# Kernel tuning notes

Hardware: AMD Instinct MI355X
Metric: run time of the kernel (lower is better)

The kernel has to match this reference:

```python
import jax, jax.numpy as jnp
import numpy as np
from jax import lax

DN = ('NCHW', 'OIHW', 'NCHW')

def _conv(x, w, pad):
    return lax.conv_general_dilated(x, w, (1, 1), pad, dimension_numbers=DN)

def _bn(x, p, eps=1e-5):
    # p: [4, C] rows = gamma, beta, mean, var ; inference-mode batchnorm
    g, b, m, v = p[0], p[1], p[2], p[3]
    scale = g / jnp.sqrt(v + eps)
    return (x - m[:, None, None]) * scale[:, None, None] + b[:, None, None]

def setup_inputs() -> dict:
    key = jax.random.key(0)
    ks = jax.random.split(key, 12)
    B, C, H, W = 16, 512, 56, 56
    mid = C // 2
    def bn_params(k):
        k1, k2, k3, k4 = jax.random.split(k, 4)
        g = 1.0 + 0.1 * jax.random.normal(k1, (mid,), jnp.float32)
        b = 0.1 * jax.random.normal(k2, (mid,), jnp.float32)
        m = 0.1 * jax.random.normal(k3, (mid,), jnp.float32)
        v = 0.5 + jax.random.uniform(k4, (mid,), jnp.float32)
        return jnp.stack([g, b, m, v])
    return {
        'x': jax.random.normal(ks[0], (B, C, H, W), jnp.float32),
        'w_main': 0.03 * jax.random.normal(ks[1], (mid, C, 3, 3), jnp.float32),
        'w_1x1': 0.05 * jax.random.normal(ks[2], (mid, C, 1, 1), jnp.float32),
        'w31': 0.05 * jax.random.normal(ks[3], (mid, C, 1, 1), jnp.float32),
        'bn31': bn_params(ks[4]),
        'w33': 0.05 * jax.random.normal(ks[5], (mid, mid, 3, 3), jnp.float32),
        'bn33': bn_params(ks[6]),
        'wa1': 0.05 * jax.random.normal(ks[7], (mid, C, 1, 1), jnp.float32),
        'bna1': bn_params(ks[8]),
        'bna2': bn_params(ks[9]),
        'fuse_weight': jnp.ones((4,), jnp.float32),
        'c_score': jax.random.normal(ks[10], (2 * C,), jnp.float32),
    }

def reference(x, w_main, w_1x1, w31, bn31, w33, bn33, wa1, bna1, bna2, fuse_weight, c_score):
    c = x.shape[1]
    # four branches (note: forward applies BN only inside the 3x3 and avg branches)
    acs_main = _conv(x * fuse_weight[0], w_main, 'SAME')
    acs_1x1 = _conv(x * fuse_weight[1], w_1x1, 'VALID')
    acs_3x3 = _bn(_conv(_bn(_conv(x * fuse_weight[2], w31, 'VALID'), bn31), w33, 'SAME'), bn33)
    avg_in = _bn(_conv(x * fuse_weight[3], wa1, 'VALID'), bna1)
    # AvgPool2d(k=3, s=1, p=1, count_include_pad=True)
    pooled = lax.reduce_window(avg_in, 0.0, lax.add, (1, 1, 3, 3), (1, 1, 1, 1),
                               [(0, 0), (0, 0), (1, 1), (1, 1)]) / 9.0
    acs_avg = _bn(pooled, bna2)
    out = jnp.concatenate([acs_main, acs_1x1, acs_3x3, acs_avg], axis=1)  # [B, 2c, H, W]
    # sparse 1x1 selection: output channel i = input channel ind[i] * sigmoid(c_score[ind[i]])
    _, ind = lax.top_k(c_score, c)
    scale = jax.nn.sigmoid(c_score)[ind]  # [c]
    out = out[:, ind] * scale[None, :, None, None]
    return out
```

## Files before the change

kernel.cpp:

```cpp
#include <hip/hip_runtime.h>
#include <hip/hip_bf16.h>
#include <cstdint>
#include <cstddef>

typedef _Float16 f16x8_t __attribute__((ext_vector_type(8)));
typedef float    f32x4_t __attribute__((ext_vector_type(4)));
typedef unsigned short u16x8_t __attribute__((ext_vector_type(8)));
typedef unsigned short u16x4_t __attribute__((ext_vector_type(4)));

__device__ __forceinline__ unsigned short f2h(float f) {
    return __builtin_bit_cast(unsigned short, (_Float16)f);
}
__device__ __forceinline__ float h2f(unsigned short h) {
    return (float)__builtin_bit_cast(_Float16, h);
}
__device__ __forceinline__ f16x8_t load_h8(const unsigned short* p) {
    u16x8_t r = *(const u16x8_t*)p;
    return __builtin_bit_cast(f16x8_t, r);
}

#define BATCH 16
#define CFULL 512
#define CMID  256
#define HW    3136
#define WDIM  56

#define POS_STRIDE_SH 40
#define LDS_SHORTS (348 * 40)

__global__ void prep_tabs(const float* __restrict__ cscore,
                          const float* __restrict__ bn31, const float* __restrict__ bn33,
                          const float* __restrict__ bna1, const float* __restrict__ bna2,
                          int* __restrict__ pos_tab, float* __restrict__ scale_tab,
                          float* __restrict__ bnab)
{
    __shared__ float s[1024];
    int t = threadIdx.x;
    s[t] = cscore[t];
    __syncthreads();
    float sj = s[t];
    int cnt = 0;
    for (int k = 0; k < 1024; ++k) {
        float sk = s[k];
        cnt += (sk > sj) || (sk == sj && k < t);
    }
    pos_tab[t]   = (cnt < 512) ? cnt : -1;
    scale_tab[t] = 1.0f / (1.0f + expf(-sj));

    if (t < 256) {
        const float* srcs[4] = {bn31, bn33, bna1, bna2};
        #pragma unroll
        for (int q = 0; q < 4; ++q) {
            const float* sp = srcs[q];
            float g = sp[t], b = sp[256 + t], m = sp[512 + t], v = sp[768 + t];
            float a = g * rsqrtf(v + 1e-5f);
            bnab[q * 512 + t]       = a;
            bnab[q * 512 + 256 + t] = b - m * a;
        }
    }
}

__global__ void prep_weights(const float* __restrict__ w_main, const float* __restrict__ w_1x1,
                             const float* __restrict__ w31, const float* __restrict__ wa1,
                             const float* __restrict__ w33, const float* __restrict__ fw,
                             unsigned short* __restrict__ Wcat,
                             unsigned short* __restrict__ Wmain,
                             unsigned short* __restrict__ W33r)
{
    int i = blockIdx.x * 256 + threadIdx.x;
    if (i < 393216) {
        int row = i >> 9, c = i & 511;
        float v;
        if (row < 256)      v = w_1x1[row * 512 + c] * fw[1];
        else if (row < 512) v = w31[(row - 256) * 512 + c] * fw[2];
        else                v = wa1[(row - 512) * 512 + c] * fw[3];
        Wcat[((c >> 5) * 768 + row) * 32 + (c & 31)] = f2h(v);
    } else if (i < 393216 + 1179648) {
        int j = i - 393216;
        int o = j / 4608, r = j % 4608, tap = r >> 9, c = r & 511;
        Wmain[(((c >> 5) * 9 + tap) * 256 + o) * 32 + (c & 31)] =
            f2h(w_main[(size_t)(o * 512 + c) * 9 + tap] * fw[0]);
    } else if (i < 2162688) {
        int j = i - 1572864;
        int o = j / 2304, r = j % 2304, tap = r >> 8, c = r & 255;
        W33r[(((c >> 5) * 9 + tap) * 256 + o) * 32 + (c & 31)] =
            f2h(w33[(size_t)(o * 256 + c) * 9 + tap]);
    }
}

__global__ void transpose_x(const float* __restrict__ x, unsigned short* __restrict__ xt)
{
    __shared__ unsigned short tile[64][65];
    int t = threadIdx.x;
    int hw0 = blockIdx.x * 64, c0 = blockIdx.y * 64, b = blockIdx.z;
    const float* xb = x + ((size_t)b * CFULL + c0) * HW + hw0;
    int hwL = t & 63, cL = t >> 6;
    #pragma unroll
    for (int i = 0; i < 16; ++i) {
        int c = cL + i * 4;
        tile[c][hwL] = f2h(xb[(size_t)c * HW + hwL]);
    }
    __syncthreads();
    int c8 = (t & 7) * 8, hw = t >> 3;
    #pragma unroll
    for (int i = 0; i < 2; ++i) {
        int hh = hw + i * 32;
        u16x8_t v;
        #pragma unroll
        for (int j = 0; j < 8; ++j) v[j] = tile[c8 + j][hh];
        *(u16x8_t*)(xt + ((size_t)b * HW + hw0 + hh) * CFULL + c0 + c8) = v;
    }
}

template<int CIN, int NTAP, int MODE>
__device__ __forceinline__ void conv_body(
    const unsigned short* __restrict__ X,
    const unsigned short* __restrict__ Wr,
    float* __restrict__ out,
    unsigned short* __restrict__ u_dst,
    unsigned short* __restrict__ avg_dst,
    const float* __restrict__ bnab,
    const int* __restrict__ pos_tab,
    const float* __restrict__ scale_tab,
    unsigned short* smem, int b, int ob, int pb)
{
    const int t    = threadIdx.x;
    const int lane = t & 63;
    const int wid  = t >> 6;
    const int wm = wid >> 1, wn = wid & 1;
    const int lr = lane & 15;
    const int ko = (lane >> 4) * 8;
    const int row0 = pb * 4;

    const int o_wave = ob * 128 + wm * 64;
    const int p_wave = pb * 224 + wn * 112;

    int bofs[7];
    #pragma unroll
    for (int n = 0; n < 7; ++n) {
        int p = p_wave + n * 16 + lr;
        bofs[n] = ((p / WDIM - row0) * 58 + p % WDIM) * POS_STRIDE_SH + ko;
    }

    const int r_lo = (NTAP == 9) ? 0 : 1;
    const int nitems = ((NTAP == 9) ? 6 : 4) * 224;
    int  s_src[6];
    int  s_dst[6];
    bool s_val[6];
    #pragma unroll
    for (int i = 0; i < 6; ++i) {
        int idx = t + i * 256;
        bool act = idx < nitems;
        int r   = r_lo + idx / 224;
        int rm  = idx % 224;
        int col = rm >> 2, sub = rm & 3;
        int ir  = row0 + r - 1;
        s_val[i] = act && ((unsigned)ir < (unsigned)WDIM);
        s_src[i] = (ir * WDIM + col) * CIN + sub * 8;
        s_dst[i] = (r * 58 + col + 1) * POS_STRIDE_SH + sub * 8;
    }

    #pragma unroll
    for (int i = 0; i < 7; ++i) {
        int j = t + i * 256;
        if (j < LDS_SHORTS / 8)
            *(u16x8_t*)(smem + j * 8) = (u16x8_t){0, 0, 0, 0, 0, 0, 0, 0};
    }

    f32x4_t acc[4][7];
    #pragma unroll
    for (int m = 0; m < 4; ++m)
        #pragma unroll
        for (int n = 0; n < 7; ++n)
            acc[m][n] = (f32x4_t){0.f, 0.f, 0.f, 0.f};

    const int astep = (MODE == 1) ? 768 * 32 : 256 * 32;
    const unsigned short* am[4];
    #pragma unroll
    for (int m = 0; m < 4; ++m)
        am[m] = Wr + (size_t)(o_wave + m * 16 + lr) * 32 + ko;

    const unsigned short* xb = X + (size_t)b * HW * CIN;
    const int KCH = CIN / 32;

    for (int kch = 0; kch < KCH; ++kch) {
        __syncthreads();
        u16x8_t buf[6];
        #pragma unroll
        for (int i = 0; i < 6; ++i)
            if (s_val[i]) buf[i] = *(const u16x8_t*)(xb + s_src[i] + kch * 32);
        #pragma unroll
        for (int i = 0; i < 6; ++i)
            if (s_val[i]) *(u16x8_t*)(smem + s_dst[i]) = buf[i];
        __syncthreads();

        #pragma unroll
        for (int tap = 0; tap < NTAP; ++tap) {
            const int toff = (NTAP == 9) ? (((tap / 3) * 58 + tap % 3) * POS_STRIDE_SH)
                                         : (59 * POS_STRIDE_SH);
            f16x8_t af[4];
            #pragma unroll
            for (int m = 0; m < 4; ++m)
                af[m] = load_h8(am[m] + (size_t)(kch * NTAP + tap) * astep);
            f16x8_t bf[7];
            #pragma unroll
            for (int n = 0; n < 7; ++n)
                bf[n] = load_h8(smem + bofs[n] + toff);
            __builtin_amdgcn_s_setprio(1);
            #pragma unroll
            for (int m = 0; m < 4; ++m)
                #pragma unroll
                for (int n = 0; n < 7; ++n)
                    acc[m][n] = __builtin_amdgcn_mfma_f32_16x16x32_f16(af[m], bf[n], acc[m][n], 0, 0, 0);
            __builtin_amdgcn_s_setprio(0);
        }
    }

    const int fq = lane >> 4;
    const int seg = (MODE == 1) ? (ob >> 1) : 0;
    const bool bn_write = (MODE == 1) && (seg != 0);

    #pragma unroll
    for (int m = 0; m < 4; ++m) {
        const int orow = o_wave + m * 16 + fq * 4;
        #pragma unroll
        for (int n = 0; n < 7; ++n) {
            const int p = p_wave + n * 16 + lr;
            f32x4_t v = acc[m][n];
            if (bn_write) {
                const int lc0 = orow - seg * 256;
                const float* ab = (seg == 1) ? (bnab + 0 * 512) : (bnab + 2 * 512);
                unsigned short* dst = (seg == 1) ? u_dst : avg_dst;
                u16x4_t pk;
                #pragma unroll
                for (int j = 0; j < 4; ++j) {
                    float a = ab[lc0 + j], bb = ab[256 + lc0 + j];
                    pk[j] = f2h(a * v[j] + bb);
                }
                *(u16x4_t*)(dst + ((size_t)b * HW + p) * CMID + lc0) = pk;
            } else {
                const int cbase = (MODE == 0) ? 0 : ((MODE == 2) ? 512 : 256);
                #pragma unroll
                for (int j = 0; j < 4; ++j) {
                    int o = orow + j;
                    float val2 = v[j];
                    if (MODE == 2) val2 = bnab[512 + o] * val2 + bnab[512 + 256 + o];
                    int jc = cbase + o;
                    int pos = pos_tab[jc];
                    if (pos >= 0)
                        out[((size_t)b * CFULL + pos) * HW + p] = val2 * scale_tab[jc];
                }
            }
        }
    }
}

__global__ __launch_bounds__(256, 2)
void fusedK(const unsigned short* __restrict__ X,
            const unsigned short* __restrict__ Wcat,
            float* __restrict__ out,
            unsigned short* __restrict__ u_dst,
            unsigned short* __restrict__ avg_dst,
            const float* __restrict__ bnab,
            const int* __restrict__ pos_tab,
            const float* __restrict__ scale_tab)
{
    __shared__ unsigned short smem[LDS_SHORTS];
    const int id = blockIdx.x;
    const int xcd = id & 7, slot = id >> 3;
    const int b = xcd + 8 * (slot / 84);
    const int u = slot % 84;
    conv_body<512, 1, 1>(X, Wcat, out, u_dst, avg_dst, bnab,
                         pos_tab, scale_tab, smem, b, u / 14, u % 14);
}

__global__ __launch_bounds__(256, 2)
void longK(const unsigned short* __restrict__ X,
           const unsigned short* __restrict__ Wmain,
           const unsigned short* __restrict__ U,
           const unsigned short* __restrict__ W33r,
           const unsigned short* __restrict__ avgin,
           float* __restrict__ out,
           const float* __restrict__ bnab,
           const int* __restrict__ pos_tab,
           const float* __restrict__ scale_tab)
{
    __shared__ unsigned short smem[LDS_SHORTS];
    const int id = blockIdx.x;
    const int xcd = id & 7, slot = id >> 3;
    if (slot < 112) {
        const int b = xcd + 8 * (slot / 56);
        const int rr = slot % 56;
        const int idx = rr >> 1;
        const int ob = idx / 14, pb = idx % 14;
        if ((rr & 1) == 0)
            conv_body<512, 9, 0>(X, Wmain, out, nullptr, nullptr, bnab,
                                 pos_tab, scale_tab, smem, b, ob, pb);
        else
            conv_body<256, 9, 2>(U, W33r, out, nullptr, nullptr, bnab,
                                 pos_tab, scale_tab, smem, b, ob, pb);
    } else {
        const int s2 = slot - 112;
        const int b = xcd + 8 * (s2 / 392);
        const int q = s2 % 392;
        const int t = threadIdx.x;
        const int p = q * 8 + (t >> 5);
        const int c0 = (t & 31) * 8;
        const int h = p / WDIM, w = p % WDIM;
        const float* ab2 = bnab + 3 * 512;
        float s[8];
        #pragma unroll
        for (int j = 0; j < 8; ++j) s[j] = 0.f;
        #pragma unroll
        for (int dh = -1; dh <= 1; ++dh) {
            int hh = h + dh;
            if ((unsigned)hh >= (unsigned)WDIM) continue;
            #pragma unroll
            for (int dw = -1; dw <= 1; ++dw) {
                int ww = w + dw;
                if ((unsigned)ww >= (unsigned)WDIM) continue;
                u16x8_t v = *(const u16x8_t*)(avgin + ((size_t)b * HW + hh * WDIM + ww) * CMID + c0);
                #pragma unroll
                for (int j = 0; j < 8; ++j) s[j] += h2f(v[j]);
            }
        }
        #pragma unroll
        for (int j = 0; j < 8; ++j) {
            int c = c0 + j;
            int jc = 768 + c;
            int pos = pos_tab[jc];
            if (pos >= 0) {
                float val = (s[j] * (1.f / 9.f)) * ab2[c] + ab2[256 + c];
                out[((size_t)b * CFULL + pos) * HW + p] = val * scale_tab[jc];
            }
        }
    }
}

extern "C" void kernel_launch(void* const* d_in, const int* in_sizes, int n_in,
                              void* d_out, int out_size, void* d_ws, size_t ws_size,
                              hipStream_t stream) {
    (void)in_sizes; (void)n_in; (void)out_size; (void)ws_size;
    const float* x      = (const float*)d_in[0];
    const float* w_main = (const float*)d_in[1];
    const float* w_1x1  = (const float*)d_in[2];
    const float* w31    = (const float*)d_in[3];
    const float* bn31   = (const float*)d_in[4];
    const float* w33    = (const float*)d_in[5];
    const float* bn33   = (const float*)d_in[6];
    const float* wa1    = (const float*)d_in[7];
    const float* bna1   = (const float*)d_in[8];
    const float* bna2   = (const float*)d_in[9];
    const float* fw     = (const float*)d_in[10];
    const float* cscore = (const float*)d_in[11];
    float* out = (float*)d_out;

    char* ws = (char*)d_ws;
    unsigned short* x_nhwc = (unsigned short*)(ws);
    unsigned short* u_nhwc = (unsigned short*)(ws + 51380224);
    unsigned short* avgin  = (unsigned short*)(ws + 77070336);
    unsigned short* Wcat   = (unsigned short*)(ws + 102760448);
    unsigned short* Wmain  = (unsigned short*)(ws + 103546880);
    unsigned short* W33r   = (unsigned short*)(ws + 105906176);
    float*          bnab   = (float*)        (ws + 107085824);
    int*            pos_tab= (int*)          (ws + 107094016);
    float*          scl_tab= (float*)        (ws + 107098112);

    dim3 blk(256);

    prep_tabs<<<dim3(1), dim3(1024), 0, stream>>>(cscore, bn31, bn33, bna1, bna2,
                                                  pos_tab, scl_tab, bnab);
    prep_weights<<<dim3(8448), blk, 0, stream>>>(w_main, w_1x1, w31, wa1, w33, fw,
                                                 Wcat, Wmain, W33r);
    transpose_x<<<dim3(49, 8, 16), blk, 0, stream>>>(x, x_nhwc);

    fusedK<<<dim3(1344), blk, 0, stream>>>(x_nhwc, Wcat, out,
                                           u_nhwc, avgin, bnab, pos_tab, scl_tab);

    longK<<<dim3(7168), blk, 0, stream>>>(x_nhwc, Wmain, u_nhwc, W33r, avgin,
                                          out, bnab, pos_tab, scl_tab);
}
```

Measured before the change: 435.9 us.

## Add double-buffered software-pipelined 3x3 conv path with prefetched weights

Adds a new conv_sched routine for the two 3x3 convolutions in longK. It double-buffers the input halo tile in LDS and prefetches the next channel chunk into registers during tap 7. It also register-prefetches the next tap's weight fragments and uses explicit waitcnt, sched_barrier and setprio so the MFMAs overlap the loads. The longK LDS allocation doubles plus a dump region, which may cut occupancy below the two blocks per CU requested.

```diff
diff --git a/kernel.cpp b/kernel.cpp
--- a/kernel.cpp
+++ b/kernel.cpp
@@ -255,6 +255,161 @@
     }
 }
 
+template<int CIN, int MODE>
+__device__ __forceinline__ void conv_sched(
+    const unsigned short* __restrict__ X,
+    const unsigned short* __restrict__ Wr,
+    float* __restrict__ out,
+    const float* __restrict__ bnab,
+    const int* __restrict__ pos_tab,
+    const float* __restrict__ scale_tab,
+    unsigned short* smem, int b, int ob, int pb)
+{
+    const int t    = threadIdx.x;
+    const int lane = t & 63;
+    const int wid  = t >> 6;
+    const int wm = wid >> 1, wn = wid & 1;
+    const int lr = lane & 15;
+    const int ko = (lane >> 4) * 8;
+    const int row0 = pb * 4;
+
+    const int o_wave = ob * 128 + wm * 64;
+    const int p_wave = pb * 224 + wn * 112;
+
+    int bofs[7];
+    #pragma unroll
+    for (int n = 0; n < 7; ++n) {
+        int p = p_wave + n * 16 + lr;
+        bofs[n] = ((p / WDIM - row0) * 58 + p % WDIM) * POS_STRIDE_SH + ko;
+    }
+
+    const int nitems = 6 * 224;
+    const int dump_off = 2 * LDS_SHORTS + (t & 63) * 8 + (wid & 3) * 512;
+    int s_src[6];
+    int s_dst[6];
+    #pragma unroll
+    for (int i = 0; i < 6; ++i) {
+        int idx = t + i * 256;
+        int r   = idx / 224;
+        int rm  = idx % 224;
+        int col = rm >> 2, sub = rm & 3;
+        int ir  = row0 + r - 1;
+        bool v  = (idx < nitems) && ((unsigned)ir < (unsigned)WDIM);
+        int ir_c = v ? ir : 0;
+        s_src[i] = (ir_c * WDIM + col) * CIN + sub * 8;
+        s_dst[i] = v ? ((r * 58 + col + 1) * POS_STRIDE_SH + sub * 8) : dump_off;
+    }
+
+    #pragma unroll
+    for (int i = 0; i < 14; ++i) {
+        int j = t + i * 256;
+        if (j < 2 * LDS_SHORTS / 8)
+            *(u16x8_t*)(smem + j * 8) = (u16x8_t){0, 0, 0, 0, 0, 0, 0, 0};
+    }
+
+    f32x4_t acc[4][7];
+    #pragma unroll
+    for (int m = 0; m < 4; ++m)
+        #pragma unroll
+        for (int n = 0; n < 7; ++n)
+            acc[m][n] = (f32x4_t){0.f, 0.f, 0.f, 0.f};
+
+    const int astep = 256 * 32;
+    const unsigned short* am[4];
+    #pragma unroll
+    for (int m = 0; m < 4; ++m)
+        am[m] = Wr + (size_t)(o_wave + m * 16 + lr) * 32 + ko;
+
+    const unsigned short* xb = X + (size_t)b * HW * CIN;
+    const int KCH = CIN / 32;
+
+    u16x8_t sbuf[6];
+    __syncthreads();
+    #pragma unroll
+    for (int i = 0; i < 6; ++i)
+        sbuf[i] = *(const u16x8_t*)(xb + s_src[i]);
+    asm volatile("s_waitcnt vmcnt(0)" ::: "memory");
+    #pragma unroll
+    for (int i = 0; i < 6; ++i)
+        *(u16x8_t*)(smem + s_dst[i]) = sbuf[i];
+    f16x8_t afc[4], afn[4];
+    #pragma unroll
+    for (int m = 0; m < 4; ++m)
+        afc[m] = load_h8(am[m]);
+    asm volatile("s_waitcnt lgkmcnt(0)" ::: "memory");
+    __builtin_amdgcn_s_barrier();
+
+    #pragma unroll 1
+    for (int kch = 0; kch < KCH; ++kch) {
+        const unsigned short* rbuf = smem + (kch & 1) * LDS_SHORTS;
+        unsigned short* wbuf = smem + ((kch + 1) & 1) * LDS_SHORTS;
+        const int nk = (kch + 1 < KCH) ? (kch + 1) : 0;
+
+        #pragma unroll
+        for (int tap = 0; tap < 9; ++tap) {
+            int kt = kch * 9 + tap + 1;
+            kt = (kt == KCH * 9) ? 0 : kt;
+            #pragma unroll
+            for (int m = 0; m < 4; ++m)
+                afn[m] = load_h8(am[m] + (size_t)kt * astep);
+            if (tap == 7) {
+                #pragma unroll
+                for (int i = 0; i < 6; ++i)
+                    sbuf[i] = *(const u16x8_t*)(xb + s_src[i] + nk * 32);
+            }
+            const int toff = ((tap / 3) * 58 + tap % 3) * POS_STRIDE_SH;
+            f16x8_t bf[7];
+            #pragma unroll
+            for (int n = 0; n < 7; ++n)
+                bf[n] = load_h8(rbuf + bofs[n] + toff);
+            if (tap < 7)
+                asm volatile("s_waitcnt vmcnt(4) lgkmcnt(0)" ::: "memory");
+            else
+                asm volatile("s_waitcnt vmcnt(10) lgkmcnt(0)" ::: "memory");
+            __builtin_amdgcn_sched_barrier(0);
+            __builtin_amdgcn_s_setprio(1);
+            #pragma unroll
+            for (int m = 0; m < 4; ++m)
+                #pragma unroll
+                for (int n = 0; n < 7; ++n)
+                    acc[m][n] = __builtin_amdgcn_mfma_f32_16x16x32_f16(afc[m], bf[n], acc[m][n], 0, 0, 0);
+            __builtin_amdgcn_s_setprio(0);
+            __builtin_amdgcn_sched_barrier(0);
+            #pragma unroll
+            for (int m = 0; m < 4; ++m) afc[m] = afn[m];
+        }
+
+        asm volatile("s_waitcnt vmcnt(4)" ::: "memory");
+        #pragma unroll
+        for (int i = 0; i < 6; ++i)
+            *(u16x8_t*)(wbuf + s_dst[i]) = sbuf[i];
+        asm volatile("s_waitcnt lgkmcnt(0)" ::: "memory");
+        __builtin_amdgcn_s_barrier();
+    }
+
+    const int fq = lane >> 4;
+    #pragma unroll
+    for (int m = 0; m < 4; ++m) {
+        const int orow = o_wave + m * 16 + fq * 4;
+        #pragma unroll
+        for (int n = 0; n < 7; ++n) {
+            const int p = p_wave + n * 16 + lr;
+            f32x4_t v = acc[m][n];
+            const int cbase = (MODE == 0) ? 0 : 512;
+            #pragma unroll
+            for (int j = 0; j < 4; ++j) {
+                int o = orow + j;
+                float val2 = v[j];
+                if (MODE == 2) val2 = bnab[512 + o] * val2 + bnab[512 + 256 + o];
+                int jc = cbase + o;
+                int pos = pos_tab[jc];
+                if (pos >= 0)
+                    out[((size_t)b * CFULL + pos) * HW + p] = val2 * scale_tab[jc];
+            }
+        }
+    }
+}
+
 __global__ __launch_bounds__(256, 2)
 void fusedK(const unsigned short* __restrict__ X,
             const unsigned short* __restrict__ Wcat,
@@ -285,7 +440,7 @@
            const int* __restrict__ pos_tab,
            const float* __restrict__ scale_tab)
 {
-    __shared__ unsigned short smem[LDS_SHORTS];
+    __shared__ unsigned short smem[2 * LDS_SHORTS + 2048];
     const int id = blockIdx.x;
     const int xcd = id & 7, slot = id >> 3;
     if (slot < 112) {
@@ -294,11 +449,9 @@
         const int idx = rr >> 1;
         const int ob = idx / 14, pb = idx % 14;
         if ((rr & 1) == 0)
-            conv_body<512, 9, 0>(X, Wmain, out, nullptr, nullptr, bnab,
-                                 pos_tab, scale_tab, smem, b, ob, pb);
+            conv_sched<512, 0>(X, Wmain, out, bnab, pos_tab, scale_tab, smem, b, ob, pb);
         else
-            conv_body<256, 9, 2>(U, W33r, out, nullptr, nullptr, bnab,
-                                 pos_tab, scale_tab, smem, b, ob, pb);
+            conv_sched<256, 2>(U, W33r, out, bnab, pos_tab, scale_tab, smem, b, ob, pb);
     } else {
         const int s2 = slot - 112;
         const int b = xcd + 8 * (s2 / 392);
```

Measured after the change: 420.5 us. 3.5% less time.
